# Kernel tuning notes

Measured on AMD Instinct MI355X. Metric: run time of the kernel, lower is better.

## Reference

```python
import jax, jax.numpy as jnp
import numpy as np

N = 4096          # total atoms
N_METAL = 1024    # first N_METAL atoms are metal (Z=79) by construction
L = 24.0          # cubic cell edge (Angstrom)
DL = 2.4
NK = 10           # int(L / DL) -- static k-grid extent per axis
SIGMA = 1.0 / 1.805132
SCALING = 1.0
FOUR_PI = 4.0 * np.pi

# static integer reciprocal grid with k=0 removed: (K,3), K = (2*NK+1)^3 - 1
_g = np.arange(-NK, NK + 1)
_INTS = np.stack(np.meshgrid(_g, _g, _g, indexing="ij"), axis=-1).reshape(-1, 3)
_INTS = _INTS[np.any(_INTS != 0, axis=1)].astype(np.float32)


def _ewald_potential(r, q, cell):
    """Reciprocal-space Ewald potential at each atom position.
    r: (n,3) positions, q: (n,m) charges (m charge columns), cell: (3,3)
    rows = lattice vectors. Returns (n,m) potential ('field' f in cace).
    pot_i = (4*pi/V) * sum_k exp(-sigma^2 k^2/2)/k^2 * Re[S(k) e^{-ik.r_i}]."""
    recip = (2.0 * np.pi) * jnp.linalg.inv(cell).T      # rows b1,b2,b3
    k = jnp.asarray(_INTS, dtype=r.dtype) @ recip       # (K,3)
    k2 = jnp.sum(k * k, axis=1)                         # (K,)
    kfac = jnp.exp((-0.5 * SIGMA * SIGMA) * k2) / k2    # (K,)
    vol = jnp.abs(jnp.linalg.det(cell))
    kr = r @ k.T                                        # (n,K)  dominant alloc
    c, s = jnp.cos(kr), jnp.sin(kr)
    sf_c = c.T @ q                                      # (K,m) structure factors
    sf_s = s.T @ q
    pot = c @ (kfac[:, None] * sf_c) + s @ (kfac[:, None] * sf_s)
    return (FOUR_PI / vol) * pot


def setup_inputs() -> dict:
    key = jax.random.key(0)
    k1, k2 = jax.random.split(key)
    positions = jax.random.uniform(k1, (N, 3), dtype=jnp.float32) * L
    q = jax.random.normal(k2, (N, 1), dtype=jnp.float32) * 0.1
    cell = (L * jnp.eye(3, dtype=jnp.float32)).reshape(1, 3, 3)
    atomic_numbers = jnp.concatenate([
        jnp.full((N_METAL,), 79, dtype=jnp.int32),   # metal block first
        jnp.full((N - N_METAL,), 8, dtype=jnp.int32),
    ])
    batch = jnp.zeros((N,), dtype=jnp.int32)         # single system
    return {"positions": positions, "q": q, "cell": cell,
            "atomic_numbers": atomic_numbers, "batch": batch}


def reference(positions, q, cell, atomic_numbers, batch):
    # single batch (batch all zeros); metal atoms are the first N_METAL
    # (atomic_numbers == 79 by construction, so the boolean mask is static)
    cell0 = cell.reshape(3, 3)
    q = q.at[:N_METAL].set(0.0)                      # q_all[metal] = 0
    r_m = positions[:N_METAL]

    # _compute_S_matrix: pairwise Ewald kernel among metal atoms via q=eye
    A = _ewald_potential(r_m, jnp.eye(N_METAL, dtype=positions.dtype), cell0)
    coeffs = jnp.ones((N_METAL + 1, N_METAL + 1), dtype=positions.dtype)
    coeffs = coeffs.at[:N_METAL, :N_METAL].set(A)
    coeffs = coeffs.at[N_METAL, N_METAL].set(0.0)
    S = jnp.linalg.inv(coeffs)                       # cached AJl in torch code

    # field at every atom from all (electrolyte) charges
    f = _ewald_potential(positions, q, cell0)        # (N,1)

    # external_field is None -> B_ext = 0, no external energy
    B = -f[:N_METAL] * SCALING                       # (N_METAL,1)
    chi = jnp.concatenate([B, jnp.zeros((1, 1), dtype=B.dtype)], axis=0)
    sol = S @ chi                                    # (N_METAL+1,1)
    q_mw = q.at[:N_METAL].set(sol[:-1] / SCALING)
    return q_mw
```

## Files before the change

kernel.cpp:

```cpp
#include <hip/hip_runtime.h>
#include <math.h>

#define NATOM 4096
#define NM    1024
#define NKR   9260
#define KSPLIT 14
#define CHPS  22
#define NCH   308
#define KC    32
#define KPAD2 9856
#define PI_F  3.14159265358979f

typedef short v8s __attribute__((ext_vector_type(8)));
typedef float v4f __attribute__((ext_vector_type(4)));

static __device__ __forceinline__ void kdata(int t, const float* __restrict__ cell,
                                             float& kxx, float& kyy, float& kzz, float& w) {
  if (t >= NKR) { kxx = 0.f; kyy = 0.f; kzz = 0.f; w = 0.f; return; }
  int u = (t < 4630) ? t : t + 1;
  int a = u / 441;
  int rem = u - a * 441;
  int b = rem / 21;
  int c = rem - b * 21;
  float na = (float)(a - 10), nb = (float)(b - 10), nc = (float)(c - 10);
  float m00=cell[0], m01=cell[1], m02=cell[2];
  float m10=cell[3], m11=cell[4], m12=cell[5];
  float m20=cell[6], m21=cell[7], m22=cell[8];
  float det = m00*(m11*m22 - m12*m21) - m01*(m10*m22 - m12*m20) + m02*(m10*m21 - m11*m20);
  float inv00 =  (m11*m22 - m12*m21) / det;
  float inv01 = -(m01*m22 - m02*m21) / det;
  float inv02 =  (m01*m12 - m02*m11) / det;
  float inv10 = -(m10*m22 - m12*m20) / det;
  float inv11 =  (m00*m22 - m02*m20) / det;
  float inv12 = -(m00*m12 - m02*m10) / det;
  float inv20 =  (m10*m21 - m11*m20) / det;
  float inv21 = -(m00*m21 - m01*m20) / det;
  float inv22 =  (m00*m11 - m01*m10) / det;
  const float twopi = 2.f * PI_F;
  kxx = twopi * (na*inv00 + nb*inv01 + nc*inv02);
  kyy = twopi * (na*inv10 + nb*inv11 + nc*inv12);
  kzz = twopi * (na*inv20 + nb*inv21 + nc*inv22);
  float k2 = kxx*kxx + kyy*kyy + kzz*kzz;
  const float sigma = 1.0f / 1.805132f;
  w = (4.f * PI_F / fabsf(det)) * __expf(-0.5f * sigma * sigma * k2) / k2;
}

__global__ __launch_bounds__(256)
void sfk(const float* __restrict__ pos, const float* __restrict__ q,
         const float* __restrict__ cell,
         float* __restrict__ kx, float* __restrict__ ky,
         float* __restrict__ kz, float* __restrict__ ksw,
         float* __restrict__ gc, float* __restrict__ gs) {
  __shared__ float red1[8][32], red2[8][32];
  const int kloc = threadIdx.x & 31;
  const int part = threadIdx.x >> 5;
  const int k = blockIdx.x * 32 + kloc;
  float kxx, kyy, kzz, w;
  kdata(k, cell, kxx, kyy, kzz, w);
  if (part == 0) { kx[k]=kxx; ky[k]=kyy; kz[k]=kzz; ksw[k]=sqrtf(w); }
  float sc = 0.f, ss = 0.f;
  const int j0 = NM + part * 384, j1 = j0 + 384;
  for (int j = j0; j < j1; ++j) {
    float kr = kxx*pos[3*j] + kyy*pos[3*j+1] + kzz*pos[3*j+2];
    float s, c;
    __sincosf(kr, &s, &c);
    float qj = q[j];
    sc += qj * c;
    ss += qj * s;
  }
  red1[part][kloc] = sc;
  red2[part][kloc] = ss;
  __syncthreads();
  if (part == 0) {
    float tc = 0.f, ts = 0.f;
    #pragma unroll
    for (int pp = 0; pp < 8; ++pp) { tc += red1[pp][kloc]; ts += red2[pp][kloc]; }
    gc[k] = w * tc;
    gs[k] = w * ts;
  }
}

__global__ __launch_bounds__(256)
void fB(const float* __restrict__ pos,
        const float* __restrict__ kx, const float* __restrict__ ky,
        const float* __restrict__ kz,
        const float* __restrict__ gc, const float* __restrict__ gs,
        float* __restrict__ r1, float* __restrict__ r2) {
  int i = blockIdx.x;
  float px = pos[3*i], py = pos[3*i+1], pz = pos[3*i+2];
  float p = 0.f;
  for (int k = threadIdx.x; k < KPAD2; k += 256) {
    float kr = kx[k]*px + ky[k]*py + kz[k]*pz;
    float s, c;
    __sincosf(kr, &s, &c);
    p += gc[k]*c + gs[k]*s;
  }
  for (int o = 32; o > 0; o >>= 1) p += __shfl_down(p, o, 64);
  __shared__ float red[4];
  if ((threadIdx.x & 63) == 0) red[threadIdx.x >> 6] = p;
  __syncthreads();
  if (threadIdx.x == 0) {
    r1[i] = -(red[0] + red[1] + red[2] + red[3]);
    r2[i] = 1.f;
  }
}

#define PSTR 40
__global__ __launch_bounds__(256, 2)
void gemmA(const float* __restrict__ pos,
           const float* __restrict__ kx, const float* __restrict__ ky,
           const float* __restrict__ kz, const float* __restrict__ ksw,
           float* __restrict__ A) {
  __shared__ short Pl[8][128 * PSTR];
  const int blk = blockIdx.x;
  const int split = blk / 36;
  const int tt = blk - split * 36;
  int bi = 0, rem = tt;
  while (rem >= 8 - bi) { rem -= 8 - bi; ++bi; }
  const int bj = bi + rem;
  const int t = threadIdx.x;
  const int side = t >> 7;
  const int a = t & 127;
  const int atom = (side ? bj : bi) * 128 + a;
  const float px = pos[3*atom], py = pos[3*atom+1], pz = pos[3*atom+2];
  const int axor = (a >> 3) & 3;
  short* PC_hi = &Pl[side*4+0][a*PSTR];
  short* PC_mi = &Pl[side*4+1][a*PSTR];
  short* PS_hi = &Pl[side*4+2][a*PSTR];
  short* PS_mi = &Pl[side*4+3][a*PSTR];

  const int w = t >> 6;
  const int lane = t & 63;
  const int ln15 = lane & 15;
  const int quad = lane >> 4;

  v4f acc[2][8];
  #pragma unroll
  for (int mt = 0; mt < 2; ++mt)
    #pragma unroll
    for (int nt = 0; nt < 8; ++nt) {
      v4f z = {0.f, 0.f, 0.f, 0.f};
      acc[mt][nt] = z;
    }

  for (int ch = split * CHPS; ch < split * CHPS + CHPS; ++ch) {
    const int kb = ch * KC;
    #pragma unroll
    for (int g = 0; g < 4; ++g) {
      v8s vch, vcm, vsh, vsm;
      #pragma unroll
      for (int j = 0; j < 8; ++j) {
        const int gk = kb + g*8 + j;
        float kr = kx[gk]*px + ky[gk]*py + kz[gk]*pz;
        float s, c;
        __sincosf(kr, &s, &c);
        float sw = ksw[gk];
        float cv = c * sw, sv = s * sw;
        unsigned cu = __float_as_uint(cv);
        float chf = __uint_as_float(cu & 0xffff0000u);
        unsigned cmu = __float_as_uint(cv - chf);
        unsigned su = __float_as_uint(sv);
        float shf = __uint_as_float(su & 0xffff0000u);
        unsigned smu = __float_as_uint(sv - shf);
        vch[j] = (short)(cu >> 16);
        vcm[j] = (short)(cmu >> 16);
        vsh[j] = (short)(su >> 16);
        vsm[j] = (short)(smu >> 16);
      }
      const int slot = (g ^ axor) * 8;
      *(v8s*)&PC_hi[slot] = vch;
      *(v8s*)&PC_mi[slot] = vcm;
      *(v8s*)&PS_hi[slot] = vsh;
      *(v8s*)&PS_mi[slot] = vsm;
    }
    __syncthreads();
    v8s aCh[2], aCm[2], aSh[2], aSm[2];
    #pragma unroll
    for (int mt = 0; mt < 2; ++mt) {
      const int row = w*32 + mt*16 + ln15;
      const int off = row * PSTR + (quad ^ ((row >> 3) & 3)) * 8;
      aCh[mt] = *(const v8s*)&Pl[0][off];
      aCm[mt] = *(const v8s*)&Pl[1][off];
      aSh[mt] = *(const v8s*)&Pl[2][off];
      aSm[mt] = *(const v8s*)&Pl[3][off];
    }
    #pragma unroll
    for (int nt = 0; nt < 8; ++nt) {
      const int row = nt*16 + ln15;
      const int off = row * PSTR + (quad ^ ((row >> 3) & 3)) * 8;
      v8s bCh = *(const v8s*)&Pl[4][off];
      v8s bCm = *(const v8s*)&Pl[5][off];
      v8s bSh = *(const v8s*)&Pl[6][off];
      v8s bSm = *(const v8s*)&Pl[7][off];
      #pragma unroll
      for (int mt = 0; mt < 2; ++mt) {
        v4f d = acc[mt][nt];
        d = __builtin_amdgcn_mfma_f32_16x16x32_bf16(aCh[mt], bCh, d, 0, 0, 0);
        d = __builtin_amdgcn_mfma_f32_16x16x32_bf16(aCh[mt], bCm, d, 0, 0, 0);
        d = __builtin_amdgcn_mfma_f32_16x16x32_bf16(aCm[mt], bCh, d, 0, 0, 0);
        d = __builtin_amdgcn_mfma_f32_16x16x32_bf16(aSh[mt], bSh, d, 0, 0, 0);
        d = __builtin_amdgcn_mfma_f32_16x16x32_bf16(aSh[mt], bSm, d, 0, 0, 0);
        d = __builtin_amdgcn_mfma_f32_16x16x32_bf16(aSm[mt], bSh, d, 0, 0, 0);
        acc[mt][nt] = d;
      }
    }
    __syncthreads();
  }
  #pragma unroll
  for (int mt = 0; mt < 2; ++mt)
    #pragma unroll
    for (int nt = 0; nt < 8; ++nt)
      #pragma unroll
      for (int r = 0; r < 4; ++r) {
        const int row = bi*128 + w*32 + mt*16 + quad*4 + r;
        const int col = bj*128 + nt*16 + ln15;
        atomicAdd(&A[row*1024 + col], acc[mt][nt][r]);
      }
}

__global__ __launch_bounds__(256)
void step(float* __restrict__ A, const float* __restrict__ r1, const float* __restrict__ r2,
          float* __restrict__ ru1, float* __restrict__ ru2,
          float* __restrict__ y1g, float* __restrict__ y2g, int p) {
  __shared__ __align__(16) float D[32][36];
  __shared__ __align__(16) float T[32][36];
  __shared__ float y1s[32], y2s[32];
  const int t = threadIdx.x;
  const int nb = 32 - p;
  const int i0 = (t >> 4) * 2, j0 = (t & 15) * 2;
  const int lr = t >> 3, lc = (t & 7) * 4;

  if ((int)blockIdx.x >= nb) {
    int rem = blockIdx.x - nb, a = 0;
    while (rem >= a + 1) { rem -= (a + 1); ++a; }
    const int qi = p + 1 + a, qj = p + 1 + rem;
    *(v4f*)&D[lr][lc] = *(const v4f*)&A[(qi*32+lr)*1024 + (p-1)*32 + lc];
    *(v4f*)&T[lr][lc] = *(const v4f*)&A[(qj*32+lr)*1024 + (p-1)*32 + lc];
    float o[2][2];
    if (p == 1 && (qi >> 2) != (qj >> 2)) {
      #pragma unroll
      for (int ii = 0; ii < 2; ++ii)
        #pragma unroll
        for (int jj = 0; jj < 2; ++jj)
          o[ii][jj] = A[(qj*32 + j0+jj)*1024 + qi*32 + i0+ii];
    } else {
      #pragma unroll
      for (int ii = 0; ii < 2; ++ii)
        #pragma unroll
        for (int jj = 0; jj < 2; ++jj)
          o[ii][jj] = A[(qi*32+i0+ii)*1024 + qj*32 + j0+jj];
    }
    __syncthreads();
    for (int m = 0; m < 32; ++m) {
      float a0 = D[i0][m], a1 = D[i0+1][m];
      float b0 = T[j0][m], b1 = T[j0+1][m];
      o[0][0]-=a0*b0; o[0][1]-=a0*b1;
      o[1][0]-=a1*b0; o[1][1]-=a1*b1;
    }
    #pragma unroll
    for (int ii = 0; ii < 2; ++ii)
      #pragma unroll
      for (int jj = 0; jj < 2; ++jj)
        A[(qi*32+i0+ii)*1024 + qj*32 + j0+jj] = o[ii][jj];
    return;
  }

  const int b = blockIdx.x;
  const int q = p + b;
  if (p == 0) {
    *(v4f*)&D[lr][lc] = *(const v4f*)&A[lr*1024 + lc];
    if (b > 0) {
      if (q < 4) {
        *(v4f*)&T[lr][lc] = *(const v4f*)&A[(q*32+lr)*1024 + lc];
      } else {
        for (int e = t; e < 1024; e += 256)
          T[e&31][e>>5] = A[(e>>5)*1024 + q*32 + (e&31)];
      }
    }
    __syncthreads();
  } else {
    *(v4f*)&D[lr][lc] = *(const v4f*)&A[(p*32+lr)*1024 + (p-1)*32 + lc];
    if (b > 0)
      *(v4f*)&T[lr][lc] = *(const v4f*)&A[(q*32+lr)*1024 + (p-1)*32 + lc];
    __syncthreads();
    float o1[2][2];
    #pragma unroll
    for (int ii = 0; ii < 2; ++ii)
      #pragma unroll
      for (int jj = 0; jj < 2; ++jj)
        o1[ii][jj] = A[(p*32+i0+ii)*1024 + p*32 + j0+jj];
    for (int m = 0; m < 32; ++m) {
      float a0 = D[i0][m], a1 = D[i0+1][m];
      float b0 = D[j0][m], b1 = D[j0+1][m];
      o1[0][0]-=a0*b0; o1[0][1]-=a0*b1;
      o1[1][0]-=a1*b0; o1[1][1]-=a1*b1;
    }
    float o2[2][2];
    if (b > 0) {
      if (p == 1 && (q >> 2) != 0) {
        #pragma unroll
        for (int ii = 0; ii < 2; ++ii)
          #pragma unroll
          for (int jj = 0; jj < 2; ++jj)
            o2[ii][jj] = A[(1*32 + j0+jj)*1024 + q*32 + i0+ii];
      } else {
        #pragma unroll
        for (int ii = 0; ii < 2; ++ii)
          #pragma unroll
          for (int jj = 0; jj < 2; ++jj)
            o2[ii][jj] = A[(q*32+i0+ii)*1024 + p*32 + j0+jj];
      }
      for (int m = 0; m < 32; ++m) {
        float a0 = T[i0][m], a1 = T[i0+1][m];
        float b0 = D[j0][m], b1 = D[j0+1][m];
        o2[0][0]-=a0*b0; o2[0][1]-=a0*b1;
        o2[1][0]-=a1*b0; o2[1][1]-=a1*b1;
      }
    }
    __syncthreads();
    #pragma unroll
    for (int ii = 0; ii < 2; ++ii)
      #pragma unroll
      for (int jj = 0; jj < 2; ++jj)
        D[i0+ii][j0+jj] = o1[ii][jj];
    if (b > 0) {
      #pragma unroll
      for (int ii = 0; ii < 2; ++ii)
        #pragma unroll
        for (int jj = 0; jj < 2; ++jj)
          T[i0+ii][j0+jj] = o2[ii][jj];
    }
    __syncthreads();
  }

  if (t < 32) {
    float a[32];
    #pragma unroll
    for (int m = 0; m < 32; ++m) a[m] = D[t][m];
    #pragma unroll
    for (int j = 0; j < 32; ++j) {
      float dj = __shfl(a[j], j);
      float rinv = rsqrtf(dj);
      float lj = (t == j) ? dj * rinv : a[j] * rinv;
      a[j] = lj;
      #pragma unroll
      for (int m = j + 1; m < 32; ++m)
        a[m] -= lj * __shfl(lj, m);
    }
    #pragma unroll
    for (int m = 0; m < 32; ++m) D[t][m] = a[m];
  }
  __syncthreads();
  if (b == 0) {
    for (int e = t; e < 1024; e += 256) {
      int i = e >> 5, j = e & 31;
      if (i >= j) A[(p*32+i)*1024 + p*32 + j] = D[i][j];
    }
  } else {
    if (t < 32) {
      #pragma unroll
      for (int cb = 0; cb < 2; ++cb) {
        const int cbase = cb * 16;
        float x[16];
        #pragma unroll
        for (int k = 0; k < 16; ++k) x[k] = T[t][cbase + k];
        for (int m = 0; m < cbase; ++m) {
          float tm = T[t][m];
          #pragma unroll
          for (int k = 0; k < 16; ++k)
            x[k] -= tm * D[cbase + k][m];
        }
        #pragma unroll
        for (int k = 0; k < 16; ++k) {
          float xv = x[k] * (1.0f / D[cbase + k][cbase + k]);
          x[k] = xv;
          #pragma unroll
          for (int m2 = k + 1; m2 < 16; ++m2)
            x[m2] -= xv * D[cbase + m2][cbase + k];
        }
        #pragma unroll
        for (int k = 0; k < 16; ++k) T[t][cbase + k] = x[k];
      }
    }
    __syncthreads();
    *(v4f*)&A[(q*32+lr)*1024 + p*32 + lc] = *(const v4f*)&T[lr][lc];
  }
  __syncthreads();
  if (t < 32) {
    float v1 = r1[p*32 + t], v2 = r2[p*32 + t];
    for (int j = 0; j < 32; ++j) {
      float invd = 1.f / D[j][j];
      float Lij = D[t][j];
      float x1 = __shfl(v1, j) * invd;
      float x2 = __shfl(v2, j) * invd;
      if (t == j)      { v1 = x1; v2 = x2; }
      else if (t > j)  { v1 -= Lij * x1; v2 -= Lij * x2; }
    }
    y1s[t] = v1; y2s[t] = v2;
    if (b == 0) { y1g[p*32 + t] = v1; y2g[p*32 + t] = v2; }
  }
  __syncthreads();
  if (b > 0 && t < 32) {
    float a1 = 0.f, a2 = 0.f;
    for (int j = 0; j < 32; ++j) {
      float lv = T[t][j];
      a1 += lv * y1s[j];
      a2 += lv * y2s[j];
    }
    ru1[q*32 + t] -= a1;
    ru2[q*32 + t] -= a2;
  }
}

__global__ __launch_bounds__(64)
void invd(const float* __restrict__ A, float* __restrict__ iD) {
  __shared__ float Lb[64][65];
  __shared__ float Xs[64][65];
  const int k = blockIdx.x;
  const int j = threadIdx.x;
  const int base = k * 64;
  for (int e = j; e < 4096; e += 64) {
    int r = e >> 6, c = e & 63;
    Lb[r][c] = (r >= c) ? A[(base + r)*1024 + base + c] : 0.f;
  }
  __syncthreads();
  for (int r = 0; r < j; ++r) Xs[r][j] = 0.f;
  Xs[j][j] = 1.f / Lb[j][j];
  for (int r = j + 1; r < 64; ++r) {
    float s = 0.f;
    for (int m = j; m < r; ++m) s += Lb[r][m] * Xs[m][j];
    Xs[r][j] = -s / Lb[r][r];
  }
  __syncthreads();
  for (int e = j; e < 4096; e += 64)
    iD[k*4096 + e] = Xs[e>>6][e&63];
}

__global__ __launch_bounds__(1024)
void bwd_out(const float* __restrict__ A, const float* __restrict__ iD,
             float* __restrict__ y1g, float* __restrict__ y2g,
             const float* __restrict__ qin, float* __restrict__ out) {
  __shared__ float D[64][65];
  __shared__ float yin1[64], yin2[64];
  __shared__ float x1s[64], x2s[64];
  __shared__ float rs1[16], rs2[16];
  const int t = threadIdx.x;
  for (int p = 15; p >= 0; --p) {
    const int base = p * 64;
    for (int e = t; e < 4096; e += 1024)
      D[e>>6][e&63] = iD[p*4096 + e];
    if (t < 64) { yin1[t] = y1g[base + t]; yin2[t] = y2g[base + t]; }
    __syncthreads();
    if (t < 64) {
      float v1 = 0.f, v2 = 0.f;
      #pragma unroll 8
      for (int m = 0; m < 64; ++m) {
        float w = D[m][t];
        v1 += w * yin1[m];
        v2 += w * yin2[m];
      }
      y1g[base + t] = v1; y2g[base + t] = v2;
      x1s[t] = v1; x2s[t] = v2;
    }
    __syncthreads();
    for (int rr = t; rr < base; rr += 1024) {
      float a1 = 0.f, a2 = 0.f;
      #pragma unroll 8
      for (int jj = 0; jj < 64; ++jj) {
        float lv = A[(base+jj)*1024 + rr];
        a1 += lv * x1s[jj];
        a2 += lv * x2s[jj];
      }
      y1g[rr] -= a1; y2g[rr] -= a2;
    }
    __syncthreads();
  }
  float s1 = y1g[t], s2 = y2g[t];
  for (int o = 32; o > 0; o >>= 1) { s1 += __shfl_down(s1, o, 64); s2 += __shfl_down(s2, o, 64); }
  if ((t & 63) == 0) { rs1[t >> 6] = s1; rs2[t >> 6] = s2; }
  __syncthreads();
  if (t == 0) {
    float a = 0.f, bb = 0.f;
    #pragma unroll
    for (int w = 0; w < 16; ++w) { a += rs1[w]; bb += rs2[w]; }
    rs1[0] = a / bb;
  }
  __syncthreads();
  const float lam = rs1[0];
  out[t] = y1g[t] - lam * y2g[t];
  for (int e = NM + t; e < NATOM; e += 1024) out[e] = qin[e];
}

extern "C" void kernel_launch(void* const* d_in, const int* in_sizes, int n_in,
                              void* d_out, int out_size, void* d_ws, size_t ws_size,
                              hipStream_t stream) {
  const float* pos  = (const float*)d_in[0];
  const float* q    = (const float*)d_in[1];
  const float* cell = (const float*)d_in[2];
  float* out = (float*)d_out;

  float* ws  = (float*)d_ws;
  float* A   = ws;
  float* kx  = ws + 1048576;
  float* ky  = kx + KPAD2;
  float* kz  = ky + KPAD2;
  float* ksw = kz + KPAD2;
  float* gc  = ksw + KPAD2;
  float* gs  = gc + KPAD2;
  float* r1  = gs + KPAD2;
  float* r2  = r1 + 1024;
  float* y1g = r2 + 1024;
  float* y2g = y1g + 1024;
  float* iD  = y2g + 1024;

  sfk<<<NCH, 256, 0, stream>>>(pos, q, cell, kx, ky, kz, ksw, gc, gs);
  fB<<<NM, 256, 0, stream>>>(pos, kx, ky, kz, gc, gs, r1, r2);
  hipMemsetAsync(A, 0, 1024 * 1024 * sizeof(float), stream);
  gemmA<<<36 * KSPLIT, 256, 0, stream>>>(pos, kx, ky, kz, ksw, A);
  for (int p = 0; p < 32; ++p) {
    const int s = 31 - p;
    const int grid = (32 - p) + ((p >= 1) ? s * (s + 1) / 2 : 0);
    step<<<grid, 256, 0, stream>>>(A, r1, r2, r1, r2, y1g, y2g, p);
  }
  invd<<<16, 64, 0, stream>>>(A, iD);
  bwd_out<<<1, 1024, 0, stream>>>(A, iD, y1g, y2g, q, out);
}
```

Measured before the change: 885.7 us.

## Enlarge Cholesky panel block from 32 to 64 to halve step launches

The blocked Cholesky and forward solve now use 64x64 tiles instead of 32x32, so the step kernel is launched 16 times instead of 32. The diagonal block is factored as two 32-wide Cholesky sub-blocks with a TRSM and Schur update between them, and each thread now updates a 4x4 output tile. This cuts launch count and serial dependency steps, in exchange for fewer, heavier blocks per launch, more serial single-warp work on the diagonal, larger shared memory, and scalar instead of vectorized loads.

```diff
diff --git a/kernel.cpp b/kernel.cpp
--- a/kernel.cpp
+++ b/kernel.cpp
@@ -218,177 +218,221 @@
       }
 }
 
+static __device__ __forceinline__ void chol32(float (*Dl)[65], int r0, int c0, int t) {
+  float a[32];
+  #pragma unroll
+  for (int m = 0; m < 32; ++m) a[m] = Dl[r0 + t][c0 + m];
+  #pragma unroll
+  for (int j = 0; j < 32; ++j) {
+    float dj = __shfl(a[j], j);
+    float rinv = rsqrtf(dj);
+    float lj = (t == j) ? dj * rinv : a[j] * rinv;
+    a[j] = lj;
+    #pragma unroll
+    for (int m = j + 1; m < 32; ++m)
+      a[m] -= lj * __shfl(lj, m);
+  }
+  #pragma unroll
+  for (int m = 0; m < 32; ++m) Dl[r0 + t][c0 + m] = a[m];
+}
+
+static __device__ __forceinline__ void trsm_row(float* row, const float (*Lm)[65], int ncb) {
+  for (int cb = 0; cb < ncb; ++cb) {
+    const int cbase = cb * 16;
+    float x[16];
+    #pragma unroll
+    for (int k = 0; k < 16; ++k) x[k] = row[cbase + k];
+    for (int m = 0; m < cbase; ++m) {
+      float tm = row[m];
+      #pragma unroll
+      for (int k = 0; k < 16; ++k)
+        x[k] -= tm * Lm[cbase + k][m];
+    }
+    #pragma unroll
+    for (int k = 0; k < 16; ++k) {
+      float xv = x[k] * (1.0f / Lm[cbase + k][cbase + k]);
+      x[k] = xv;
+      #pragma unroll
+      for (int m2 = k + 1; m2 < 16; ++m2)
+        x[m2] -= xv * Lm[cbase + m2][cbase + k];
+    }
+    #pragma unroll
+    for (int k = 0; k < 16; ++k) row[cbase + k] = x[k];
+  }
+}
+
 __global__ __launch_bounds__(256)
 void step(float* __restrict__ A, const float* __restrict__ r1, const float* __restrict__ r2,
           float* __restrict__ ru1, float* __restrict__ ru2,
           float* __restrict__ y1g, float* __restrict__ y2g, int p) {
-  __shared__ __align__(16) float D[32][36];
-  __shared__ __align__(16) float T[32][36];
-  __shared__ float y1s[32], y2s[32];
+  __shared__ float D[64][65];
+  __shared__ float T[64][65];
+  __shared__ float y1s[64], y2s[64];
   const int t = threadIdx.x;
-  const int nb = 32 - p;
-  const int i0 = (t >> 4) * 2, j0 = (t & 15) * 2;
-  const int lr = t >> 3, lc = (t & 7) * 4;
+  const int nb = 16 - p;
+  const int i0 = (t >> 4) * 4, j0 = (t & 15) * 4;
 
   if ((int)blockIdx.x >= nb) {
-    int rem = blockIdx.x - nb, a = 0;
-    while (rem >= a + 1) { rem -= (a + 1); ++a; }
-    const int qi = p + 1 + a, qj = p + 1 + rem;
-    *(v4f*)&D[lr][lc] = *(const v4f*)&A[(qi*32+lr)*1024 + (p-1)*32 + lc];
-    *(v4f*)&T[lr][lc] = *(const v4f*)&A[(qj*32+lr)*1024 + (p-1)*32 + lc];
-    float o[2][2];
-    if (p == 1 && (qi >> 2) != (qj >> 2)) {
-      #pragma unroll
-      for (int ii = 0; ii < 2; ++ii)
+    int rem = blockIdx.x - nb, aa = 0;
+    while (rem >= aa + 1) { rem -= (aa + 1); ++aa; }
+    const int qi = p + 1 + aa, qj = p + 1 + rem;
+    for (int e = t; e < 4096; e += 256) {
+      int r = e >> 6, c = e & 63;
+      D[r][c] = A[(qi*64 + r)*1024 + (p-1)*64 + c];
+      T[r][c] = A[(qj*64 + r)*1024 + (p-1)*64 + c];
+    }
+    float o[4][4];
+    if (p == 1 && (qi >> 1) != (qj >> 1)) {
+      #pragma unroll
+      for (int ii = 0; ii < 4; ++ii)
         #pragma unroll
-        for (int jj = 0; jj < 2; ++jj)
-          o[ii][jj] = A[(qj*32 + j0+jj)*1024 + qi*32 + i0+ii];
+        for (int jj = 0; jj < 4; ++jj)
+          o[ii][jj] = A[(qj*64 + j0+jj)*1024 + qi*64 + i0+ii];
     } else {
       #pragma unroll
-      for (int ii = 0; ii < 2; ++ii)
+      for (int ii = 0; ii < 4; ++ii)
         #pragma unroll
-        for (int jj = 0; jj < 2; ++jj)
-          o[ii][jj] = A[(qi*32+i0+ii)*1024 + qj*32 + j0+jj];
-    }
-    __syncthreads();
-    for (int m = 0; m < 32; ++m) {
-      float a0 = D[i0][m], a1 = D[i0+1][m];
-      float b0 = T[j0][m], b1 = T[j0+1][m];
-      o[0][0]-=a0*b0; o[0][1]-=a0*b1;
-      o[1][0]-=a1*b0; o[1][1]-=a1*b1;
-    }
-    #pragma unroll
-    for (int ii = 0; ii < 2; ++ii)
-      #pragma unroll
-      for (int jj = 0; jj < 2; ++jj)
-        A[(qi*32+i0+ii)*1024 + qj*32 + j0+jj] = o[ii][jj];
+        for (int jj = 0; jj < 4; ++jj)
+          o[ii][jj] = A[(qi*64 + i0+ii)*1024 + qj*64 + j0+jj];
+    }
+    __syncthreads();
+    for (int m = 0; m < 64; ++m) {
+      float a0 = D[i0][m], a1 = D[i0+1][m], a2 = D[i0+2][m], a3 = D[i0+3][m];
+      float b0 = T[j0][m], b1 = T[j0+1][m], b2 = T[j0+2][m], b3 = T[j0+3][m];
+      o[0][0]-=a0*b0; o[0][1]-=a0*b1; o[0][2]-=a0*b2; o[0][3]-=a0*b3;
+      o[1][0]-=a1*b0; o[1][1]-=a1*b1; o[1][2]-=a1*b2; o[1][3]-=a1*b3;
+      o[2][0]-=a2*b0; o[2][1]-=a2*b1; o[2][2]-=a2*b2; o[2][3]-=a2*b3;
+      o[3][0]-=a3*b0; o[3][1]-=a3*b1; o[3][2]-=a3*b2; o[3][3]-=a3*b3;
+    }
+    #pragma unroll
+    for (int ii = 0; ii < 4; ++ii)
+      #pragma unroll
+      for (int jj = 0; jj < 4; ++jj)
+        A[(qi*64 + i0+ii)*1024 + qj*64 + j0+jj] = o[ii][jj];
     return;
   }
 
   const int b = blockIdx.x;
   const int q = p + b;
   if (p == 0) {
-    *(v4f*)&D[lr][lc] = *(const v4f*)&A[lr*1024 + lc];
+    for (int e = t; e < 4096; e += 256) {
+      int r = e >> 6, c = e & 63;
+      D[r][c] = A[r*1024 + c];
+    }
     if (b > 0) {
-      if (q < 4) {
-        *(v4f*)&T[lr][lc] = *(const v4f*)&A[(q*32+lr)*1024 + lc];
+      if (q == 1) {
+        for (int e = t; e < 4096; e += 256) {
+          int r = e >> 6, c = e & 63;
+          T[r][c] = A[(64 + r)*1024 + c];
+        }
       } else {
-        for (int e = t; e < 1024; e += 256)
-          T[e&31][e>>5] = A[(e>>5)*1024 + q*32 + (e&31)];
+        for (int e = t; e < 4096; e += 256) {
+          int r = e >> 6, c = e & 63;
+          T[c][r] = A[r*1024 + q*64 + c];
+        }
       }
     }
     __syncthreads();
   } else {
-    *(v4f*)&D[lr][lc] = *(const v4f*)&A[(p*32+lr)*1024 + (p-1)*32 + lc];
-    if (b > 0)
-      *(v4f*)&T[lr][lc] = *(const v4f*)&A[(q*32+lr)*1024 + (p-1)*32 + lc];
-    __syncthreads();
-    float o1[2][2];
-    #pragma unroll
-    for (int ii = 0; ii < 2; ++ii)
-      #pragma unroll
-      for (int jj = 0; jj < 2; ++jj)
-        o1[ii][jj] = A[(p*32+i0+ii)*1024 + p*32 + j0+jj];
-    for (int m = 0; m < 32; ++m) {
-      float a0 = D[i0][m], a1 = D[i0+1][m];
-      float b0 = D[j0][m], b1 = D[j0+1][m];
-      o1[0][0]-=a0*b0; o1[0][1]-=a0*b1;
-      o1[1][0]-=a1*b0; o1[1][1]-=a1*b1;
-    }
-    float o2[2][2];
+    for (int e = t; e < 4096; e += 256) {
+      int r = e >> 6, c = e & 63;
+      D[r][c] = A[(p*64 + r)*1024 + (p-1)*64 + c];
+      if (b > 0)
+        T[r][c] = A[(q*64 + r)*1024 + (p-1)*64 + c];
+    }
+    __syncthreads();
+    float o1[4][4];
+    #pragma unroll
+    for (int ii = 0; ii < 4; ++ii)
+      #pragma unroll
+      for (int jj = 0; jj < 4; ++jj)
+        o1[ii][jj] = A[(p*64+i0+ii)*1024 + p*64 + j0+jj];
+    for (int m = 0; m < 64; ++m) {
+      float a0 = D[i0][m], a1 = D[i0+1][m], a2 = D[i0+2][m], a3 = D[i0+3][m];
+      float b0 = D[j0][m], b1 = D[j0+1][m], b2 = D[j0+2][m], b3 = D[j0+3][m];
+      o1[0][0]-=a0*b0; o1[0][1]-=a0*b1; o1[0][2]-=a0*b2; o1[0][3]-=a0*b3;
+      o1[1][0]-=a1*b0; o1[1][1]-=a1*b1; o1[1][2]-=a1*b2; o1[1][3]-=a1*b3;
+      o1[2][0]-=a2*b0; o1[2][1]-=a2*b1; o1[2][2]-=a2*b2; o1[2][3]-=a2*b3;
+      o1[3][0]-=a3*b0; o1[3][1]-=a3*b1; o1[3][2]-=a3*b2; o1[3][3]-=a3*b3;
+    }
+    float o2[4][4];
     if (b > 0) {
-      if (p == 1 && (q >> 2) != 0) {
+      if (p == 1) {
         #pragma unroll
-        for (int ii = 0; ii < 2; ++ii)
+        for (int ii = 0; ii < 4; ++ii)
           #pragma unroll
-          for (int jj = 0; jj < 2; ++jj)
-            o2[ii][jj] = A[(1*32 + j0+jj)*1024 + q*32 + i0+ii];
+          for (int jj = 0; jj < 4; ++jj)
+            o2[ii][jj] = A[(64 + j0+jj)*1024 + q*64 + i0+ii];
       } else {
         #pragma unroll
-        for (int ii = 0; ii < 2; ++ii)
+        for (int ii = 0; ii < 4; ++ii)
           #pragma unroll
-          for (int jj = 0; jj < 2; ++jj)
-            o2[ii][jj] = A[(q*32+i0+ii)*1024 + p*32 + j0+jj];
-      }
-      for (int m = 0; m < 32; ++m) {
-        float a0 = T[i0][m], a1 = T[i0+1][m];
-        float b0 = D[j0][m], b1 = D[j0+1][m];
-        o2[0][0]-=a0*b0; o2[0][1]-=a0*b1;
-        o2[1][0]-=a1*b0; o2[1][1]-=a1*b1;
-      }
-    }
-    __syncthreads();
-    #pragma unroll
-    for (int ii = 0; ii < 2; ++ii)
-      #pragma unroll
-      for (int jj = 0; jj < 2; ++jj)
+          for (int jj = 0; jj < 4; ++jj)
+            o2[ii][jj] = A[(q*64+i0+ii)*1024 + p*64 + j0+jj];
+      }
+      for (int m = 0; m < 64; ++m) {
+        float a0 = T[i0][m], a1 = T[i0+1][m], a2 = T[i0+2][m], a3 = T[i0+3][m];
+        float b0 = D[j0][m], b1 = D[j0+1][m], b2 = D[j0+2][m], b3 = D[j0+3][m];
+        o2[0][0]-=a0*b0; o2[0][1]-=a0*b1; o2[0][2]-=a0*b2; o2[0][3]-=a0*b3;
+        o2[1][0]-=a1*b0; o2[1][1]-=a1*b1; o2[1][2]-=a1*b2; o2[1][3]-=a1*b3;
+        o2[2][0]-=a2*b0; o2[2][1]-=a2*b1; o2[2][2]-=a2*b2; o2[2][3]-=a2*b3;
+        o2[3][0]-=a3*b0; o2[3][1]-=a3*b1; o2[3][2]-=a3*b2; o2[3][3]-=a3*b3;
+      }
+    }
+    __syncthreads();
+    #pragma unroll
+    for (int ii = 0; ii < 4; ++ii)
+      #pragma unroll
+      for (int jj = 0; jj < 4; ++jj)
         D[i0+ii][j0+jj] = o1[ii][jj];
     if (b > 0) {
       #pragma unroll
-      for (int ii = 0; ii < 2; ++ii)
+      for (int ii = 0; ii < 4; ++ii)
         #pragma unroll
-        for (int jj = 0; jj < 2; ++jj)
+        for (int jj = 0; jj < 4; ++jj)
           T[i0+ii][j0+jj] = o2[ii][jj];
     }
     __syncthreads();
   }
 
-  if (t < 32) {
-    float a[32];
-    #pragma unroll
-    for (int m = 0; m < 32; ++m) a[m] = D[t][m];
-    #pragma unroll
-    for (int j = 0; j < 32; ++j) {
-      float dj = __shfl(a[j], j);
-      float rinv = rsqrtf(dj);
-      float lj = (t == j) ? dj * rinv : a[j] * rinv;
-      a[j] = lj;
-      #pragma unroll
-      for (int m = j + 1; m < 32; ++m)
-        a[m] -= lj * __shfl(lj, m);
-    }
-    #pragma unroll
-    for (int m = 0; m < 32; ++m) D[t][m] = a[m];
-  }
-  __syncthreads();
+  if (t < 32) chol32(D, 0, 0, t);
+  __syncthreads();
+  if (t < 32) trsm_row(&D[32 + t][0], D, 2);
+  __syncthreads();
+  {
+    const int si = 32 + (t >> 4) * 2, sj = 32 + (t & 15) * 2;
+    float s00 = 0.f, s01 = 0.f, s10 = 0.f, s11 = 0.f;
+    #pragma unroll
+    for (int m = 0; m < 32; ++m) {
+      float a0 = D[si][m], a1 = D[si+1][m];
+      float b0 = D[sj][m], b1 = D[sj+1][m];
+      s00 += a0*b0; s01 += a0*b1; s10 += a1*b0; s11 += a1*b1;
+    }
+    D[si][sj]   -= s00; D[si][sj+1]   -= s01;
+    D[si+1][sj] -= s10; D[si+1][sj+1] -= s11;
+  }
+  __syncthreads();
+  if (t < 32) chol32(D, 32, 32, t);
+  __syncthreads();
+
+  if (b > 0 && t < 64) trsm_row(&T[t][0], D, 4);
+  __syncthreads();
+
   if (b == 0) {
-    for (int e = t; e < 1024; e += 256) {
-      int i = e >> 5, j = e & 31;
-      if (i >= j) A[(p*32+i)*1024 + p*32 + j] = D[i][j];
+    for (int e = t; e < 4096; e += 256) {
+      int r = e >> 6, c = e & 63;
+      if (r >= c) A[(p*64 + r)*1024 + p*64 + c] = D[r][c];
     }
   } else {
-    if (t < 32) {
-      #pragma unroll
-      for (int cb = 0; cb < 2; ++cb) {
-        const int cbase = cb * 16;
-        float x[16];
-        #pragma unroll
-        for (int k = 0; k < 16; ++k) x[k] = T[t][cbase + k];
-        for (int m = 0; m < cbase; ++m) {
-          float tm = T[t][m];
-          #pragma unroll
-          for (int k = 0; k < 16; ++k)
-            x[k] -= tm * D[cbase + k][m];
-        }
-        #pragma unroll
-        for (int k = 0; k < 16; ++k) {
-          float xv = x[k] * (1.0f / D[cbase + k][cbase + k]);
-          x[k] = xv;
-          #pragma unroll
-          for (int m2 = k + 1; m2 < 16; ++m2)
-            x[m2] -= xv * D[cbase + m2][cbase + k];
-        }
-        #pragma unroll
-        for (int k = 0; k < 16; ++k) T[t][cbase + k] = x[k];
-      }
-    }
-    __syncthreads();
-    *(v4f*)&A[(q*32+lr)*1024 + p*32 + lc] = *(const v4f*)&T[lr][lc];
-  }
-  __syncthreads();
-  if (t < 32) {
-    float v1 = r1[p*32 + t], v2 = r2[p*32 + t];
-    for (int j = 0; j < 32; ++j) {
+    for (int e = t; e < 4096; e += 256) {
+      int r = e >> 6, c = e & 63;
+      A[(q*64 + r)*1024 + p*64 + c] = T[r][c];
+    }
+  }
+
+  if (t < 64) {
+    float v1 = r1[p*64 + t], v2 = r2[p*64 + t];
+    for (int j = 0; j < 64; ++j) {
       float invd = 1.f / D[j][j];
       float Lij = D[t][j];
       float x1 = __shfl(v1, j) * invd;
@@ -397,18 +441,18 @@
       else if (t > j)  { v1 -= Lij * x1; v2 -= Lij * x2; }
     }
     y1s[t] = v1; y2s[t] = v2;
-    if (b == 0) { y1g[p*32 + t] = v1; y2g[p*32 + t] = v2; }
-  }
-  __syncthreads();
-  if (b > 0 && t < 32) {
+    if (b == 0) { y1g[p*64 + t] = v1; y2g[p*64 + t] = v2; }
+  }
+  __syncthreads();
+  if (b > 0 && t < 64) {
     float a1 = 0.f, a2 = 0.f;
-    for (int j = 0; j < 32; ++j) {
+    for (int j = 0; j < 64; ++j) {
       float lv = T[t][j];
       a1 += lv * y1s[j];
       a2 += lv * y2s[j];
     }
-    ru1[q*32 + t] -= a1;
-    ru2[q*32 + t] -= a2;
+    ru1[q*64 + t] -= a1;
+    ru2[q*64 + t] -= a2;
   }
 }
 
@@ -517,9 +561,9 @@
   fB<<<NM, 256, 0, stream>>>(pos, kx, ky, kz, gc, gs, r1, r2);
   hipMemsetAsync(A, 0, 1024 * 1024 * sizeof(float), stream);
   gemmA<<<36 * KSPLIT, 256, 0, stream>>>(pos, kx, ky, kz, ksw, A);
-  for (int p = 0; p < 32; ++p) {
-    const int s = 31 - p;
-    const int grid = (32 - p) + ((p >= 1) ? s * (s + 1) / 2 : 0);
+  for (int p = 0; p < 16; ++p) {
+    const int s = 15 - p;
+    const int grid = (16 - p) + ((p >= 1) ? s * (s + 1) / 2 : 0);
     step<<<grid, 256, 0, stream>>>(A, r1, r2, r1, r2, y1g, y2g, p);
   }
   invd<<<16, 64, 0, stream>>>(A, iD);
```

Result: slower. 1.175 ms (+32.7%).

## Process two Cholesky panels per launch to halve the step-kernel count

Applied to the files above, without the earlier changes.

Replaces the 32 per-panel Cholesky/forward-solve launches with 16 launches, each factoring two 32-column panels. The next two diagonal/sub-diagonal tiles are staged through a double-buffered scratch area written by the trailing-update blocks of the previous launch. The goal is fewer kernel launches and fewer global round trips of the dependent updates. In exchange each block does more serial work and uses more shared memory (six 32x36 tiles), and the scratch handoff adds indexing complexity.

```diff
diff --git a/kernel.cpp b/kernel.cpp
--- a/kernel.cpp
+++ b/kernel.cpp
@@ -219,25 +219,106 @@
 }
 
 __global__ __launch_bounds__(256)
-void step(float* __restrict__ A, const float* __restrict__ r1, const float* __restrict__ r2,
-          float* __restrict__ ru1, float* __restrict__ ru2,
-          float* __restrict__ y1g, float* __restrict__ y2g, int p) {
-  __shared__ __align__(16) float D[32][36];
-  __shared__ __align__(16) float T[32][36];
-  __shared__ float y1s[32], y2s[32];
+void stage6(const float* __restrict__ A, float* __restrict__ scr) {
+  const int k = blockIdx.x;
+  int rt, ct;
+  if (k == 0)      { rt = 0; ct = 0; }
+  else if (k == 1) { rt = 1; ct = 0; }
+  else if (k == 2) { rt = 1; ct = 1; }
+  else if (k == 3) { rt = 2; ct = 2; }
+  else if (k == 4) { rt = 3; ct = 2; }
+  else             { rt = 3; ct = 3; }
   const int t = threadIdx.x;
-  const int nb = 32 - p;
+  const int lr = t >> 3, lc = (t & 7) * 4;
+  *(v4f*)&scr[k*1024 + lr*32 + lc] = *(const v4f*)&A[(rt*32+lr)*1024 + ct*32 + lc];
+}
+
+static __device__ __forceinline__ void chol36(float (*Dl)[36], int t) {
+  float a[32];
+  #pragma unroll
+  for (int m = 0; m < 32; ++m) a[m] = Dl[t][m];
+  #pragma unroll
+  for (int j = 0; j < 32; ++j) {
+    float dj = __shfl(a[j], j);
+    float rinv = rsqrtf(dj);
+    float lj = (t == j) ? dj * rinv : a[j] * rinv;
+    a[j] = lj;
+    #pragma unroll
+    for (int m = j + 1; m < 32; ++m)
+      a[m] -= lj * __shfl(lj, m);
+  }
+  #pragma unroll
+  for (int m = 0; m < 32; ++m) Dl[t][m] = a[m];
+}
+
+static __device__ __forceinline__ void trsm36(float* row, const float (*Lm)[36]) {
+  #pragma unroll
+  for (int cb = 0; cb < 2; ++cb) {
+    const int cbase = cb * 16;
+    float x[16];
+    #pragma unroll
+    for (int k = 0; k < 16; ++k) x[k] = row[cbase + k];
+    for (int m = 0; m < cbase; ++m) {
+      float tm = row[m];
+      #pragma unroll
+      for (int k = 0; k < 16; ++k)
+        x[k] -= tm * Lm[cbase + k][m];
+    }
+    #pragma unroll
+    for (int k = 0; k < 16; ++k) {
+      float xv = x[k] * (1.0f / Lm[cbase + k][cbase + k]);
+      x[k] = xv;
+      #pragma unroll
+      for (int m2 = k + 1; m2 < 16; ++m2)
+        x[m2] -= xv * Lm[cbase + m2][cbase + k];
+    }
+    #pragma unroll
+    for (int k = 0; k < 16; ++k) row[cbase + k] = x[k];
+  }
+}
+
+static __device__ __forceinline__ void fwd32(const float (*Dl)[36], int u, float& v1, float& v2) {
+  for (int j = 0; j < 32; ++j) {
+    float invd = 1.f / Dl[j][j];
+    float Lij = Dl[u][j];
+    float x1 = __shfl(v1, j) * invd;
+    float x2 = __shfl(v2, j) * invd;
+    if (u == j)      { v1 = x1; v2 = x2; }
+    else if (u > j)  { v1 -= Lij * x1; v2 -= Lij * x2; }
+  }
+}
+
+#define RK32(o, X, Y) \
+  for (int m_ = 0; m_ < 32; ++m_) { \
+    float xa0 = X[i0][m_], xa1 = X[i0+1][m_]; \
+    float yb0 = Y[j0][m_], yb1 = Y[j0+1][m_]; \
+    o[0][0] -= xa0*yb0; o[0][1] -= xa0*yb1; \
+    o[1][0] -= xa1*yb0; o[1][1] -= xa1*yb1; }
+
+__global__ __launch_bounds__(256)
+void step2(float* __restrict__ A, float* __restrict__ r1, float* __restrict__ r2,
+           float* __restrict__ y1g, float* __restrict__ y2g,
+           float* __restrict__ scr, int l) {
+  __shared__ __align__(16) float S[6][32][36];
+  __shared__ float yA1[32], yA2[32], yB1[32], yB2[32];
+  __shared__ float yPs1[32], yPs2[32];
+  const int t = threadIdx.x;
+  const int P = 2 * l;
+  const int nb = 32 - P;
   const int i0 = (t >> 4) * 2, j0 = (t & 15) * 2;
   const int lr = t >> 3, lc = (t & 7) * 4;
 
   if ((int)blockIdx.x >= nb) {
-    int rem = blockIdx.x - nb, a = 0;
+    const int tau = blockIdx.x - nb;
+    int rem = tau, a = 0;
     while (rem >= a + 1) { rem -= (a + 1); ++a; }
-    const int qi = p + 1 + a, qj = p + 1 + rem;
-    *(v4f*)&D[lr][lc] = *(const v4f*)&A[(qi*32+lr)*1024 + (p-1)*32 + lc];
-    *(v4f*)&T[lr][lc] = *(const v4f*)&A[(qj*32+lr)*1024 + (p-1)*32 + lc];
+    const int qi = P + 2 + a, qj = P + 2 + rem;
+    *(v4f*)&S[0][lr][lc] = *(const v4f*)&A[(qi*32+lr)*1024 + (P-2)*32 + lc];
+    *(v4f*)&S[1][lr][lc] = *(const v4f*)&A[(qi*32+lr)*1024 + (P-1)*32 + lc];
+    *(v4f*)&S[2][lr][lc] = *(const v4f*)&A[(qj*32+lr)*1024 + (P-2)*32 + lc];
+    *(v4f*)&S[3][lr][lc] = *(const v4f*)&A[(qj*32+lr)*1024 + (P-1)*32 + lc];
     float o[2][2];
-    if (p == 1 && (qi >> 2) != (qj >> 2)) {
+    if (l == 1 && (qi >> 2) != (qj >> 2)) {
       #pragma unroll
       for (int ii = 0; ii < 2; ++ii)
         #pragma unroll
@@ -251,164 +332,202 @@
           o[ii][jj] = A[(qi*32+i0+ii)*1024 + qj*32 + j0+jj];
     }
     __syncthreads();
-    for (int m = 0; m < 32; ++m) {
-      float a0 = D[i0][m], a1 = D[i0+1][m];
-      float b0 = T[j0][m], b1 = T[j0+1][m];
-      o[0][0]-=a0*b0; o[0][1]-=a0*b1;
-      o[1][0]-=a1*b0; o[1][1]-=a1*b1;
+    for (int m_ = 0; m_ < 32; ++m_) {
+      float a0 = S[0][i0][m_], a1 = S[0][i0+1][m_];
+      float c0 = S[1][i0][m_], c1 = S[1][i0+1][m_];
+      float b0 = S[2][j0][m_], b1 = S[2][j0+1][m_];
+      float d0 = S[3][j0][m_], d1 = S[3][j0+1][m_];
+      o[0][0] -= a0*b0 + c0*d0; o[0][1] -= a0*b1 + c0*d1;
+      o[1][0] -= a1*b0 + c1*d0; o[1][1] -= a1*b1 + c1*d1;
     }
     #pragma unroll
     for (int ii = 0; ii < 2; ++ii)
       #pragma unroll
       for (int jj = 0; jj < 2; ++jj)
         A[(qi*32+i0+ii)*1024 + qj*32 + j0+jj] = o[ii][jj];
-    return;
-  }
-
-  const int b = blockIdx.x;
-  const int q = p + b;
-  if (p == 0) {
-    *(v4f*)&D[lr][lc] = *(const v4f*)&A[lr*1024 + lc];
-    if (b > 0) {
-      if (q < 4) {
-        *(v4f*)&T[lr][lc] = *(const v4f*)&A[(q*32+lr)*1024 + lc];
-      } else {
-        for (int e = t; e < 1024; e += 256)
-          T[e&31][e>>5] = A[(e>>5)*1024 + q*32 + (e&31)];
-      }
-    }
-    __syncthreads();
-  } else {
-    *(v4f*)&D[lr][lc] = *(const v4f*)&A[(p*32+lr)*1024 + (p-1)*32 + lc];
-    if (b > 0)
-      *(v4f*)&T[lr][lc] = *(const v4f*)&A[(q*32+lr)*1024 + (p-1)*32 + lc];
-    __syncthreads();
-    float o1[2][2];
-    #pragma unroll
-    for (int ii = 0; ii < 2; ++ii)
-      #pragma unroll
-      for (int jj = 0; jj < 2; ++jj)
-        o1[ii][jj] = A[(p*32+i0+ii)*1024 + p*32 + j0+jj];
-    for (int m = 0; m < 32; ++m) {
-      float a0 = D[i0][m], a1 = D[i0+1][m];
-      float b0 = D[j0][m], b1 = D[j0+1][m];
-      o1[0][0]-=a0*b0; o1[0][1]-=a0*b1;
-      o1[1][0]-=a1*b0; o1[1][1]-=a1*b1;
-    }
-    float o2[2][2];
-    if (b > 0) {
-      if (p == 1 && (q >> 2) != 0) {
-        #pragma unroll
-        for (int ii = 0; ii < 2; ++ii)
-          #pragma unroll
-          for (int jj = 0; jj < 2; ++jj)
-            o2[ii][jj] = A[(1*32 + j0+jj)*1024 + q*32 + i0+ii];
-      } else {
-        #pragma unroll
-        for (int ii = 0; ii < 2; ++ii)
-          #pragma unroll
-          for (int jj = 0; jj < 2; ++jj)
-            o2[ii][jj] = A[(q*32+i0+ii)*1024 + p*32 + j0+jj];
-      }
-      for (int m = 0; m < 32; ++m) {
-        float a0 = T[i0][m], a1 = T[i0+1][m];
-        float b0 = D[j0][m], b1 = D[j0+1][m];
-        o2[0][0]-=a0*b0; o2[0][1]-=a0*b1;
-        o2[1][0]-=a1*b0; o2[1][1]-=a1*b1;
-      }
-    }
-    __syncthreads();
-    #pragma unroll
-    for (int ii = 0; ii < 2; ++ii)
-      #pragma unroll
-      for (int jj = 0; jj < 2; ++jj)
-        D[i0+ii][j0+jj] = o1[ii][jj];
-    if (b > 0) {
+    if (tau < 3) {
+      float* sd = scr + (((l + 1) & 1) * 3 + tau) * 1024;
       #pragma unroll
       for (int ii = 0; ii < 2; ++ii)
         #pragma unroll
         for (int jj = 0; jj < 2; ++jj)
-          T[i0+ii][j0+jj] = o2[ii][jj];
-    }
-    __syncthreads();
-  }
-
-  if (t < 32) {
-    float a[32];
-    #pragma unroll
-    for (int m = 0; m < 32; ++m) a[m] = D[t][m];
-    #pragma unroll
-    for (int j = 0; j < 32; ++j) {
-      float dj = __shfl(a[j], j);
-      float rinv = rsqrtf(dj);
-      float lj = (t == j) ? dj * rinv : a[j] * rinv;
-      a[j] = lj;
-      #pragma unroll
-      for (int m = j + 1; m < 32; ++m)
-        a[m] -= lj * __shfl(lj, m);
-    }
-    #pragma unroll
-    for (int m = 0; m < 32; ++m) D[t][m] = a[m];
+          sd[(i0+ii)*32 + j0+jj] = o[ii][jj];
+    }
+    return;
+  }
+
+  const int b = blockIdx.x;
+  const int q = P + b;
+  float (*LA)[36] = S[0];
+  float (*LB)[36] = S[1];
+  float (*LC)[36] = S[2];
+  float (*LD)[36] = S[3];
+  float (*Fq)[36] = S[4];
+  float (*Gq)[36] = S[5];
+
+  if (l >= 1) {
+    *(v4f*)&LA[lr][lc] = *(const v4f*)&A[(P*32+lr)*1024 + (P-2)*32 + lc];
+    *(v4f*)&LB[lr][lc] = *(const v4f*)&A[(P*32+lr)*1024 + (P-1)*32 + lc];
+    *(v4f*)&LC[lr][lc] = *(const v4f*)&A[((P+1)*32+lr)*1024 + (P-2)*32 + lc];
+    *(v4f*)&LD[lr][lc] = *(const v4f*)&A[((P+1)*32+lr)*1024 + (P-1)*32 + lc];
+    if (b >= 2) {
+      *(v4f*)&Fq[lr][lc] = *(const v4f*)&A[(q*32+lr)*1024 + (P-2)*32 + lc];
+      *(v4f*)&Gq[lr][lc] = *(const v4f*)&A[(q*32+lr)*1024 + (P-1)*32 + lc];
+    }
+    if (t < 32) {
+      yA1[t] = y1g[(P-2)*32 + t]; yA2[t] = y2g[(P-2)*32 + t];
+      yB1[t] = y1g[(P-1)*32 + t]; yB2[t] = y2g[(P-1)*32 + t];
+    }
+  }
+  __syncthreads();
+
+  const bool orig = (l <= 1);
+  const float* sc0 = scr + ((l & 1) * 3 + 0) * 1024;
+  const float* sc1 = scr + ((l & 1) * 3 + 1) * 1024;
+  const float* sc2 = scr + ((l & 1) * 3 + 2) * 1024;
+  float o0[2][2], oE[2][2], o1[2][2], oP[2][2], oQ[2][2];
+  #pragma unroll
+  for (int ii = 0; ii < 2; ++ii)
+    #pragma unroll
+    for (int jj = 0; jj < 2; ++jj) {
+      o0[ii][jj] = sc0[(i0+ii)*32 + j0+jj];
+      oE[ii][jj] = sc1[(i0+ii)*32 + j0+jj];
+      o1[ii][jj] = sc2[(i0+ii)*32 + j0+jj];
+    }
+  if (b >= 2) {
+    if (orig && (q >> 2) != (P >> 2)) {
+      #pragma unroll
+      for (int ii = 0; ii < 2; ++ii)
+        #pragma unroll
+        for (int jj = 0; jj < 2; ++jj) {
+          oP[ii][jj] = A[(P*32+j0+jj)*1024 + q*32 + i0+ii];
+          oQ[ii][jj] = A[((P+1)*32+j0+jj)*1024 + q*32 + i0+ii];
+        }
+    } else {
+      #pragma unroll
+      for (int ii = 0; ii < 2; ++ii)
+        #pragma unroll
+        for (int jj = 0; jj < 2; ++jj) {
+          oP[ii][jj] = A[(q*32+i0+ii)*1024 + P*32 + j0+jj];
+          oQ[ii][jj] = A[(q*32+i0+ii)*1024 + (P+1)*32 + j0+jj];
+        }
+    }
+  }
+  float rP1 = 0.f, rP2 = 0.f, rQ1 = 0.f, rQ2 = 0.f;
+  if (l >= 1) {
+    RK32(o0, LA, LA); RK32(o0, LB, LB);
+    RK32(oE, LC, LA); RK32(oE, LD, LB);
+    RK32(o1, LC, LC); RK32(o1, LD, LD);
+    if (b >= 2) { RK32(oP, Fq, LA); RK32(oP, Gq, LB); RK32(oQ, Fq, LC); RK32(oQ, Gq, LD); }
+    if (b >= 2 && t < 32) {
+      float a1 = 0.f, a2 = 0.f;
+      for (int j = 0; j < 32; ++j) {
+        a1 += Fq[t][j]*yA1[j] + Gq[t][j]*yB1[j];
+        a2 += Fq[t][j]*yA2[j] + Gq[t][j]*yB2[j];
+      }
+      r1[q*32 + t] -= a1; r2[q*32 + t] -= a2;
+    }
+    if (b <= 1 && t >= 128 && t < 160) {
+      const int u = t - 128;
+      float a1 = 0.f, a2 = 0.f;
+      for (int j = 0; j < 32; ++j) {
+        a1 += LA[u][j]*yA1[j] + LB[u][j]*yB1[j];
+        a2 += LA[u][j]*yA2[j] + LB[u][j]*yB2[j];
+      }
+      rP1 = r1[P*32 + u] - a1; rP2 = r2[P*32 + u] - a2;
+      if (b == 1) {
+        float c1 = 0.f, c2 = 0.f;
+        for (int j = 0; j < 32; ++j) {
+          c1 += LC[u][j]*yA1[j] + LD[u][j]*yB1[j];
+          c2 += LC[u][j]*yA2[j] + LD[u][j]*yB2[j];
+        }
+        rQ1 = r1[(P+1)*32 + u] - c1; rQ2 = r2[(P+1)*32 + u] - c2;
+      }
+    }
+  } else {
+    if (b <= 1 && t >= 128 && t < 160) {
+      const int u = t - 128;
+      rP1 = r1[u]; rP2 = r2[u];
+      if (b == 1) { rQ1 = r1[32 + u]; rQ2 = r2[32 + u]; }
+    }
+  }
+  __syncthreads();
+
+  float (*D0)[36] = S[0];
+  float (*E )[36] = S[1];
+  float (*D1)[36] = S[2];
+  float (*TP)[36] = S[3];
+  float (*TQ)[36] = S[4];
+  #pragma unroll
+  for (int ii = 0; ii < 2; ++ii)
+    #pragma unroll
+    for (int jj = 0; jj < 2; ++jj) {
+      D0[i0+ii][j0+jj] = o0[ii][jj];
+      E [i0+ii][j0+jj] = oE[ii][jj];
+    }
+  if (b >= 2)
+    #pragma unroll
+    for (int ii = 0; ii < 2; ++ii)
+      #pragma unroll
+      for (int jj = 0; jj < 2; ++jj)
+        TP[i0+ii][j0+jj] = oP[ii][jj];
+  __syncthreads();
+  if (t < 32) chol36(D0, t);
+  __syncthreads();
+  if (t < 32) trsm36(&E[t][0], (const float (*)[36])D0);
+  if (b >= 2 && t >= 64 && t < 96) trsm36(&TP[t-64][0], (const float (*)[36])D0);
+  if (b <= 1 && t >= 128 && t < 160) {
+    const int u = t - 128;
+    float v1 = rP1, v2 = rP2;
+    fwd32((const float (*)[36])D0, u, v1, v2);
+    yPs1[u] = v1; yPs2[u] = v2;
+    if (b == 0) { y1g[P*32 + u] = v1; y2g[P*32 + u] = v2; }
+  }
+  __syncthreads();
+  RK32(o1, E, E);
+  if (b >= 2) { RK32(oQ, TP, E); }
+  if (b == 1 && t >= 128 && t < 160) {
+    const int u = t - 128;
+    float a1 = 0.f, a2 = 0.f;
+    for (int j = 0; j < 32; ++j) { a1 += E[u][j]*yPs1[j]; a2 += E[u][j]*yPs2[j]; }
+    rQ1 -= a1; rQ2 -= a2;
+  }
+  #pragma unroll
+  for (int ii = 0; ii < 2; ++ii)
+    #pragma unroll
+    for (int jj = 0; jj < 2; ++jj)
+      D1[i0+ii][j0+jj] = o1[ii][jj];
+  if (b >= 2)
+    #pragma unroll
+    for (int ii = 0; ii < 2; ++ii)
+      #pragma unroll
+      for (int jj = 0; jj < 2; ++jj)
+        TQ[i0+ii][j0+jj] = oQ[ii][jj];
+  __syncthreads();
+  if (t < 32) chol36(D1, t);
+  __syncthreads();
+  if (b >= 2 && t < 32) trsm36(&TQ[t][0], (const float (*)[36])D1);
+  if (b == 1 && t >= 128 && t < 160) {
+    const int u = t - 128;
+    float v1 = rQ1, v2 = rQ2;
+    fwd32((const float (*)[36])D1, u, v1, v2);
+    y1g[(P+1)*32 + u] = v1; y2g[(P+1)*32 + u] = v2;
   }
   __syncthreads();
   if (b == 0) {
     for (int e = t; e < 1024; e += 256) {
       int i = e >> 5, j = e & 31;
-      if (i >= j) A[(p*32+i)*1024 + p*32 + j] = D[i][j];
+      if (i >= j) A[(P*32+i)*1024 + P*32 + j] = D0[i][j];
+    }
+  } else if (b == 1) {
+    *(v4f*)&A[((P+1)*32+lr)*1024 + P*32 + lc] = *(const v4f*)&E[lr][lc];
+    for (int e = t; e < 1024; e += 256) {
+      int i = e >> 5, j = e & 31;
+      if (i >= j) A[((P+1)*32+i)*1024 + (P+1)*32 + j] = D1[i][j];
     }
   } else {
-    if (t < 32) {
-      #pragma unroll
-      for (int cb = 0; cb < 2; ++cb) {
-        const int cbase = cb * 16;
-        float x[16];
-        #pragma unroll
-        for (int k = 0; k < 16; ++k) x[k] = T[t][cbase + k];
-        for (int m = 0; m < cbase; ++m) {
-          float tm = T[t][m];
-          #pragma unroll
-          for (int k = 0; k < 16; ++k)
-            x[k] -= tm * D[cbase + k][m];
-        }
-        #pragma unroll
-        for (int k = 0; k < 16; ++k) {
-          float xv = x[k] * (1.0f / D[cbase + k][cbase + k]);
-          x[k] = xv;
-          #pragma unroll
-          for (int m2 = k + 1; m2 < 16; ++m2)
-            x[m2] -= xv * D[cbase + m2][cbase + k];
-        }
-        #pragma unroll
-        for (int k = 0; k < 16; ++k) T[t][cbase + k] = x[k];
-      }
-    }
-    __syncthreads();
-    *(v4f*)&A[(q*32+lr)*1024 + p*32 + lc] = *(const v4f*)&T[lr][lc];
-  }
-  __syncthreads();
-  if (t < 32) {
-    float v1 = r1[p*32 + t], v2 = r2[p*32 + t];
-    for (int j = 0; j < 32; ++j) {
-      float invd = 1.f / D[j][j];
-      float Lij = D[t][j];
-      float x1 = __shfl(v1, j) * invd;
-      float x2 = __shfl(v2, j) * invd;
-      if (t == j)      { v1 = x1; v2 = x2; }
-      else if (t > j)  { v1 -= Lij * x1; v2 -= Lij * x2; }
-    }
-    y1s[t] = v1; y2s[t] = v2;
-    if (b == 0) { y1g[p*32 + t] = v1; y2g[p*32 + t] = v2; }
-  }
-  __syncthreads();
-  if (b > 0 && t < 32) {
-    float a1 = 0.f, a2 = 0.f;
-    for (int j = 0; j < 32; ++j) {
-      float lv = T[t][j];
-      a1 += lv * y1s[j];
-      a2 += lv * y2s[j];
-    }
-    ru1[q*32 + t] -= a1;
-    ru2[q*32 + t] -= a2;
+    *(v4f*)&A[(q*32+lr)*1024 + P*32 + lc]     = *(const v4f*)&TP[lr][lc];
+    *(v4f*)&A[(q*32+lr)*1024 + (P+1)*32 + lc] = *(const v4f*)&TQ[lr][lc];
   }
 }
 
@@ -512,15 +631,18 @@
   float* y1g = r2 + 1024;
   float* y2g = y1g + 1024;
   float* iD  = y2g + 1024;
+  float* scr = iD + 16 * 4096;
 
   sfk<<<NCH, 256, 0, stream>>>(pos, q, cell, kx, ky, kz, ksw, gc, gs);
   fB<<<NM, 256, 0, stream>>>(pos, kx, ky, kz, gc, gs, r1, r2);
   hipMemsetAsync(A, 0, 1024 * 1024 * sizeof(float), stream);
   gemmA<<<36 * KSPLIT, 256, 0, stream>>>(pos, kx, ky, kz, ksw, A);
-  for (int p = 0; p < 32; ++p) {
-    const int s = 31 - p;
-    const int grid = (32 - p) + ((p >= 1) ? s * (s + 1) / 2 : 0);
-    step<<<grid, 256, 0, stream>>>(A, r1, r2, r1, r2, y1g, y2g, p);
+  stage6<<<6, 256, 0, stream>>>(A, scr);
+  for (int l = 0; l < 16; ++l) {
+    const int nb = 32 - 2*l;
+    const int m = 30 - 2*l;
+    const int grid = nb + ((l >= 1) ? m*(m+1)/2 : 0);
+    step2<<<grid, 256, 0, stream>>>(A, r1, r2, y1g, y2g, scr, l);
   }
   invd<<<16, 64, 0, stream>>>(A, iD);
   bwd_out<<<1, 1024, 0, stream>>>(A, iD, y1g, y2g, q, out);
```

New measurement: 1.147 ms. 1.3x slower.
